# Kernel optimization log

Measured on AMD Instinct MI355X. Metric: run time of the kernel, lower is better.

The kernel has to match this reference:

```python
import jax, jax.numpy as jnp
import numpy as np

L, H, D, A, T = 2, 8, 512, 64, 256  # layers, heads, model_dim, attention_dim, target_dim
B, S = 2, 2048
EPS = 1e-5


def _ln(x, g, b):
    m = jnp.mean(x, axis=-1, keepdims=True)
    v = jnp.mean((x - m) ** 2, axis=-1, keepdims=True)
    return (x - m) / jnp.sqrt(v + EPS) * g + b


def setup_inputs() -> dict:
    key = jax.random.key(0)
    ks = jax.random.split(key, 16)
    s = 0.02
    inp = {
        "x": jax.random.normal(ks[0], (B, S, D), jnp.float32),
        # per-head QKV projections, stacked over layers and heads
        "Wq": jax.random.normal(ks[1], (L, H, D, A), jnp.float32) * s,
        "bq": jnp.zeros((L, H, A), jnp.float32),
        "Wk": jax.random.normal(ks[2], (L, H, D, A), jnp.float32) * s,
        "bk": jnp.zeros((L, H, A), jnp.float32),
        "Wv": jax.random.normal(ks[3], (L, H, D, A), jnp.float32) * s,
        "bv": jnp.zeros((L, H, A), jnp.float32),
        # output projection of concatenated heads: [H*A, D]
        "Wo": jax.random.normal(ks[4], (L, H * A, D), jnp.float32) * s,
        "bo": jnp.zeros((L, D), jnp.float32),
        # AddNorm after attention
        "ln1_g": jnp.ones((L, D), jnp.float32),
        "ln1_b": jnp.zeros((L, D), jnp.float32),
        # FFN (hidden_dim == model_dim in this module)
        "W1": jax.random.normal(ks[5], (L, D, D), jnp.float32) * s,
        "b1": jnp.zeros((L, D), jnp.float32),
        "W2": jax.random.normal(ks[6], (L, D, D), jnp.float32) * s,
        "b2": jnp.zeros((L, D), jnp.float32),
        # AddNorm after FFN
        "ln2_g": jnp.ones((L, D), jnp.float32),
        "ln2_b": jnp.zeros((L, D), jnp.float32),
        # final projection to target_dim
        "Wp": jax.random.normal(ks[7], (D, T), jnp.float32) * s,
        "bp": jnp.zeros((T,), jnp.float32),
    }
    return inp


def reference(x, Wq, bq, Wk, bk, Wv, bv, Wo, bo, ln1_g, ln1_b,
              W1, b1, W2, b2, ln2_g, ln2_b, Wp, bp):
    scale = 1.0 / jnp.sqrt(jnp.asarray(A, x.dtype))
    for i in range(L):
        # batched per-head QKV projections (math identical to per-head Linears)
        q = jnp.einsum('bsd,hda->bhsa', x, Wq[i]) + bq[i][:, None, :]
        k = jnp.einsum('bsd,hda->bhsa', x, Wk[i]) + bk[i][:, None, :]
        v = jnp.einsum('bsd,hda->bhsa', x, Wv[i]) + bv[i][:, None, :]
        scores = jnp.einsum('bhsa,bhta->bhst', q, k) * scale  # [B,H,S,S]
        attn = jax.nn.softmax(scores, axis=-1)
        heads = jnp.einsum('bhst,bhta->bhsa', attn, v)        # [B,H,S,A]
        concat = heads.transpose(0, 2, 1, 3).reshape(x.shape[0], x.shape[1], H * A)
        mha = concat @ Wo[i] + bo[i]
        x = _ln(x + mha, ln1_g[i], ln1_b[i])
        ffn = jax.nn.relu(x @ W1[i] + b1[i]) @ W2[i] + b2[i]
        x = _ln(x + ffn, ln2_g[i], ln2_b[i])
    return x @ Wp + bp
```

## Files before the change

### kernel.cpp

```cpp
#include <hip/hip_runtime.h>
#include <hip/hip_bf16.h>

#define MDIM 4096
#define DDIM 512
#define HHEADS 8
#define SLEN 2048
#define TDIM 256
#define SPLIT 4
#define LDT 66
#define LDA 66
#define EXPC 0.1803368801111244f

typedef __attribute__((ext_vector_type(8))) short short8;
typedef __attribute__((ext_vector_type(16))) float f32x16;

__device__ __forceinline__ unsigned short f2bf(float f) {
    union { __hip_bfloat16 h; unsigned short u; } c;
    c.h = __float2bfloat16(f);
    return c.u;
}
__device__ __forceinline__ float bf2f(short s) {
    return __uint_as_float((unsigned)(unsigned short)s << 16);
}

__global__ __launch_bounds__(256) void prep_k(
    const float* __restrict__ Wq, const float* __restrict__ Wk, const float* __restrict__ Wv,
    const float* __restrict__ Wo, const float* __restrict__ W1, const float* __restrict__ W2,
    const float* __restrict__ Wp, const float* __restrict__ x,
    short* __restrict__ Wqt, short* __restrict__ Wkt, short* __restrict__ Wvt,
    short* __restrict__ Wot, short* __restrict__ W1t, short* __restrict__ W2t,
    short* __restrict__ Wpt, short* __restrict__ xbf)
{
    __shared__ short T[64][72];
    const int b = blockIdx.x, tid = threadIdx.x;

    if (b >= 800) {
        const int idx = (b - 800) * 256 + tid;
        for (int e = idx; e < 262144; e += 65536) {
            float4 f0 = *(const float4*)&x[e * 8];
            float4 f1 = *(const float4*)&x[e * 8 + 4];
            short8 o;
            o[0] = (short)f2bf(f0.x); o[1] = (short)f2bf(f0.y);
            o[2] = (short)f2bf(f0.z); o[3] = (short)f2bf(f0.w);
            o[4] = (short)f2bf(f1.x); o[5] = (short)f2bf(f1.y);
            o[6] = (short)f2bf(f1.z); o[7] = (short)f2bf(f1.w);
            *(short8*)&xbf[e * 8] = o;
        }
        return;
    }

    const float* srcp; short* dstp; int ss;
    if (b < 384) {
        int w = b >> 7, t = b & 127;
        int lh = t >> 3, kt0 = (t & 7) << 6;
        const float* W = (w == 0) ? Wq : (w == 1) ? Wk : Wv;
        short* Wt = (w == 0) ? Wqt : (w == 1) ? Wkt : Wvt;
        srcp = W + (size_t)lh * 32768 + (size_t)kt0 * 64;
        dstp = Wt + (size_t)lh * 32768 + kt0;
        ss = 64;
    } else if (b < 768) {
        int w = (b - 384) >> 7, t = (b - 384) & 127;
        int l = t >> 6, tt = t & 63;
        int kt0 = (tt >> 3) << 6, nt0 = (tt & 7) << 6;
        const float* W = (w == 0) ? Wo : (w == 1) ? W1 : W2;
        short* Wt = (w == 0) ? Wot : (w == 1) ? W1t : W2t;
        srcp = W + (size_t)l * 262144 + (size_t)kt0 * 512 + nt0;
        dstp = Wt + (size_t)l * 262144 + (size_t)nt0 * 512 + kt0;
        ss = 512;
    } else {
        int t = b - 768;
        int kt0 = (t >> 2) << 6, nt0 = (t & 3) << 6;
        srcp = Wp + (size_t)kt0 * 256 + nt0;
        dstp = Wpt + (size_t)nt0 * 512 + kt0;
        ss = 256;
    }

    const int r = tid >> 2, c0 = (tid & 3) * 16;
#pragma unroll
    for (int j = 0; j < 16; j += 4) {
        float4 f = *(const float4*)&srcp[(size_t)r * ss + c0 + j];
        T[r][c0 + j + 0] = (short)f2bf(f.x);
        T[r][c0 + j + 1] = (short)f2bf(f.y);
        T[r][c0 + j + 2] = (short)f2bf(f.z);
        T[r][c0 + j + 3] = (short)f2bf(f.w);
    }
    __syncthreads();
    short8 o0, o1;
#pragma unroll
    for (int j = 0; j < 8; ++j) { o0[j] = T[c0 + j][r]; o1[j] = T[c0 + 8 + j][r]; }
    *(short8*)&dstp[(size_t)r * 512 + c0] = o0;
    *(short8*)&dstp[(size_t)r * 512 + c0 + 8] = o1;
}

__global__ __launch_bounds__(256, 2) void gemm_bf(
    const short* __restrict__ A, const short* __restrict__ Bt,
    const float* __restrict__ bias, void* __restrict__ Cout,
    int M, int N, int K, int flags)
{
    __shared__ short As[64 * LDT];
    __shared__ short Bs[64 * LDT];
    const int tid = threadIdx.x;
    const int wave = tid >> 6, lane = tid & 63;
    const int l31 = lane & 31, hi = lane >> 5;
    const int wm = wave >> 1, wn = wave & 1;
    const int m0 = blockIdx.y * 64, n0 = blockIdx.x * 64;

    f32x16 acc;
#pragma unroll
    for (int r = 0; r < 16; ++r) acc[r] = 0.f;

    const int sr = tid >> 2;
    const int sc = (tid & 3) * 16;

    for (int k0 = 0; k0 < K; k0 += 64) {
        __syncthreads();
        *(short8*)&As[sr * LDT + sc]     = *(const short8*)&A[(size_t)(m0 + sr) * K + k0 + sc];
        *(short8*)&As[sr * LDT + sc + 8] = *(const short8*)&A[(size_t)(m0 + sr) * K + k0 + sc + 8];
        *(short8*)&Bs[sr * LDT + sc]     = *(const short8*)&Bt[(size_t)(n0 + sr) * K + k0 + sc];
        *(short8*)&Bs[sr * LDT + sc + 8] = *(const short8*)&Bt[(size_t)(n0 + sr) * K + k0 + sc + 8];
        __syncthreads();

        short8 af[4], bfm[4];
#pragma unroll
        for (int ks = 0; ks < 4; ++ks) {
            af[ks]  = *(const short8*)&As[(wm * 32 + l31) * LDT + ks * 16 + hi * 8];
            bfm[ks] = *(const short8*)&Bs[(wn * 32 + l31) * LDT + ks * 16 + hi * 8];
        }
#pragma unroll
        for (int ks = 0; ks < 4; ++ks)
            acc = __builtin_amdgcn_mfma_f32_32x32x16_bf16(af[ks], bfm[ks], acc, 0, 0, 0);
    }

    const int col = n0 + wn * 32 + l31;
    const float bb = bias[col];
    const int rbase = m0 + wm * 32 + 4 * hi;
#pragma unroll
    for (int r = 0; r < 16; ++r) {
        int row = rbase + (r & 3) + 8 * (r >> 2);
        float v = acc[r] + bb;
        if (flags & 1) v = fmaxf(v, 0.f);
        if (flags & 2) ((short*)Cout)[(size_t)row * N + col] = (short)f2bf(v);
        else           ((float*)Cout)[(size_t)row * N + col] = v;
    }
}

__global__ __launch_bounds__(256, 2) void qkv_bf(
    const short* __restrict__ A,
    const short* __restrict__ Wqt, const short* __restrict__ Wkt, const short* __restrict__ Wvt,
    const float* __restrict__ bq, const float* __restrict__ bk, const float* __restrict__ bv,
    short* __restrict__ Oq, short* __restrict__ Ok, short* __restrict__ Ov)
{
    __shared__ short As[128 * LDT];
    __shared__ short Bs[64 * LDT];
    const int tid = threadIdx.x;
    const int wave = tid >> 6, lane = tid & 63;
    const int l31 = lane & 31, hi = lane >> 5;
    const int wm = wave >> 1, wn = wave & 1;
    const int m0 = blockIdx.y * 128;
    const int nt = blockIdx.x;
    const int which = nt >> 3, h = nt & 7;

    const short* Bt = ((which == 0) ? Wqt : (which == 1) ? Wkt : Wvt) + (size_t)h * 64 * 512;
    const float* bias = ((which == 0) ? bq : (which == 1) ? bk : bv) + h * 64;
    short* Out = (which == 0) ? Oq : (which == 1) ? Ok : Ov;

    f32x16 acc[2];
#pragma unroll
    for (int ms = 0; ms < 2; ++ms)
#pragma unroll
        for (int r = 0; r < 16; ++r) acc[ms][r] = 0.f;

    const int sr = tid >> 3;
    const int sc = (tid & 7) * 8;

    for (int k0 = 0; k0 < 512; k0 += 64) {
        __syncthreads();
#pragma unroll
        for (int p = 0; p < 4; ++p)
            *(short8*)&As[(p * 32 + sr) * LDT + sc] =
                *(const short8*)&A[(size_t)(m0 + p * 32 + sr) * 512 + k0 + sc];
#pragma unroll
        for (int p = 0; p < 2; ++p)
            *(short8*)&Bs[(p * 32 + sr) * LDT + sc] =
                *(const short8*)&Bt[(size_t)(p * 32 + sr) * 512 + k0 + sc];
        __syncthreads();

        short8 af[2][4], bfm[4];
#pragma unroll
        for (int ms = 0; ms < 2; ++ms)
#pragma unroll
            for (int ks = 0; ks < 4; ++ks)
                af[ms][ks] = *(const short8*)&As[(wm * 64 + ms * 32 + l31) * LDT + ks * 16 + hi * 8];
#pragma unroll
        for (int ks = 0; ks < 4; ++ks)
            bfm[ks] = *(const short8*)&Bs[(wn * 32 + l31) * LDT + ks * 16 + hi * 8];
#pragma unroll
        for (int ms = 0; ms < 2; ++ms)
#pragma unroll
            for (int ks = 0; ks < 4; ++ks)
                acc[ms] = __builtin_amdgcn_mfma_f32_32x32x16_bf16(af[ms][ks], bfm[ks], acc[ms], 0, 0, 0);
    }

    const int a = wn * 32 + l31;
    const float bb = bias[a];
    const int b = m0 >> 11;
    const int sb = (m0 & (SLEN - 1)) + wm * 64;
    const int bh = b * HHEADS + h;

    if (which == 0) {
        short* Ob = Out + (size_t)bh * SLEN * 64;
#pragma unroll
        for (int ms = 0; ms < 2; ++ms)
#pragma unroll
            for (int r = 0; r < 16; ++r) {
                int s = sb + ms * 32 + (r & 3) + 8 * (r >> 2) + 4 * hi;
                Ob[(size_t)s * 64 + a] = (short)f2bf((acc[ms][r] + bb) * EXPC);
            }
    } else if (which == 1) {
        short* Ob = Out + (size_t)bh * SLEN * 64;
#pragma unroll
        for (int ms = 0; ms < 2; ++ms)
#pragma unroll
            for (int r = 0; r < 16; ++r) {
                int s = sb + ms * 32 + (r & 3) + 8 * (r >> 2) + 4 * hi;
                Ob[(size_t)s * 64 + a] = (short)f2bf(acc[ms][r] + bb);
            }
    } else {
        short* Ob = Out + ((size_t)bh * 64 + a) * SLEN;
#pragma unroll
        for (int ms = 0; ms < 2; ++ms)
#pragma unroll
            for (int g = 0; g < 4; ++g) {
                int s = sb + ms * 32 + 8 * g + 4 * hi;
                ushort4 w;
                w.x = f2bf(acc[ms][4 * g + 0] + bb);
                w.y = f2bf(acc[ms][4 * g + 1] + bb);
                w.z = f2bf(acc[ms][4 * g + 2] + bb);
                w.w = f2bf(acc[ms][4 * g + 3] + bb);
                *(ushort4*)&Ob[s] = w;
            }
    }
}

__global__ __launch_bounds__(256, 2) void attn_mfma(
    const short* __restrict__ Qb, const short* __restrict__ Kb,
    const short* __restrict__ Vtb, short* __restrict__ Op,
    float* __restrict__ lp)
{
    __shared__ short Ks[64 * LDA];
    __shared__ short Vs[64 * LDA];

    const int tid = threadIdx.x;
    const int wid = tid >> 6;
    const int lane = tid & 63;
    const int l31 = lane & 31;
    const int hi = lane >> 5;

    const int qt = blockIdx.x;
    const int bh = blockIdx.y;
    const int sp = blockIdx.z;

    const short* Qg = Qb + (size_t)bh * SLEN * 64;
    const short* Kg = Kb + (size_t)bh * SLEN * 64;
    const short* Vg = Vtb + (size_t)bh * 64 * SLEN;

    const int q0 = qt * 256 + wid * 64;

    short8 qf[2][4];
#pragma unroll
    for (int nt = 0; nt < 2; ++nt)
#pragma unroll
        for (int ks = 0; ks < 4; ++ks)
            qf[nt][ks] = *(const short8*)&Qg[(size_t)(q0 + nt * 32 + l31) * 64 + ks * 16 + hi * 8];

    f32x16 oacc[2][2];
    float lsum[2] = {0.f, 0.f};
#pragma unroll
    for (int nt = 0; nt < 2; ++nt)
#pragma unroll
        for (int dt = 0; dt < 2; ++dt)
#pragma unroll
            for (int r = 0; r < 16; ++r) oacc[nt][dt][r] = 0.f;

    const int srow = tid >> 2;
    const int sch = (tid & 3) * 16;
    const int kbase = sp * (SLEN / SPLIT);

    short8 rk0 = *(const short8*)&Kg[(size_t)(kbase + srow) * 64 + sch];
    short8 rk1 = *(const short8*)&Kg[(size_t)(kbase + srow) * 64 + sch + 8];
    short8 rv0 = *(const short8*)&Vg[(size_t)srow * SLEN + kbase + sch];
    short8 rv1 = *(const short8*)&Vg[(size_t)srow * SLEN + kbase + sch + 8];

#pragma unroll 1
    for (int kt = 0; kt < 8; ++kt) {
        __syncthreads();
        *(short8*)&Ks[srow * LDA + sch]     = rk0;
        *(short8*)&Ks[srow * LDA + sch + 8] = rk1;
        *(short8*)&Vs[srow * LDA + sch]     = rv0;
        *(short8*)&Vs[srow * LDA + sch + 8] = rv1;
        __syncthreads();

        if (kt < 7) {
            const int k0n = kbase + (kt + 1) * 64;
            rk0 = *(const short8*)&Kg[(size_t)(k0n + srow) * 64 + sch];
            rk1 = *(const short8*)&Kg[(size_t)(k0n + srow) * 64 + sch + 8];
            rv0 = *(const short8*)&Vg[(size_t)srow * SLEN + k0n + sch];
            rv1 = *(const short8*)&Vg[(size_t)srow * SLEN + k0n + sch + 8];
        }

        short8 kf[2][4], vf[2][4];
#pragma unroll
        for (int mt = 0; mt < 2; ++mt)
#pragma unroll
            for (int ks = 0; ks < 4; ++ks)
                kf[mt][ks] = *(const short8*)&Ks[(mt * 32 + l31) * LDA + ks * 16 + hi * 8];
#pragma unroll
        for (int dt = 0; dt < 2; ++dt)
#pragma unroll
            for (int p = 0; p < 4; ++p)
                vf[dt][p] = *(const short8*)&Vs[(dt * 32 + l31) * LDA + p * 16 + hi * 8];

#pragma unroll
        for (int nt = 0; nt < 2; ++nt) {
            f32x16 sacc[2];
            __builtin_amdgcn_s_setprio(1);
#pragma unroll
            for (int mt = 0; mt < 2; ++mt) {
                f32x16 s;
#pragma unroll
                for (int r = 0; r < 16; ++r) s[r] = 0.f;
#pragma unroll
                for (int ks = 0; ks < 4; ++ks)
                    s = __builtin_amdgcn_mfma_f32_32x32x16_bf16(kf[mt][ks], qf[nt][ks], s, 0, 0, 0);
                sacc[mt] = s;
            }
            __builtin_amdgcn_s_setprio(0);

            int2 pk[2][4];
#pragma unroll
            for (int mt = 0; mt < 2; ++mt)
#pragma unroll
                for (int g = 0; g < 4; ++g) {
                    unsigned a0 = __float_as_uint(__builtin_amdgcn_exp2f(sacc[mt][4 * g + 0]));
                    unsigned a1 = __float_as_uint(__builtin_amdgcn_exp2f(sacc[mt][4 * g + 1]));
                    unsigned a2 = __float_as_uint(__builtin_amdgcn_exp2f(sacc[mt][4 * g + 2]));
                    unsigned a3 = __float_as_uint(__builtin_amdgcn_exp2f(sacc[mt][4 * g + 3]));
                    float t0 = __uint_as_float(a0 & 0xffff0000u);
                    float t1 = __uint_as_float(a1 & 0xffff0000u);
                    float t2 = __uint_as_float(a2 & 0xffff0000u);
                    float t3 = __uint_as_float(a3 & 0xffff0000u);
                    lsum[nt] += (t0 + t1) + (t2 + t3);
                    pk[mt][g].x = (int)__builtin_amdgcn_perm(a1, a0, 0x07060302u);
                    pk[mt][g].y = (int)__builtin_amdgcn_perm(a3, a2, 0x07060302u);
                }

            int2 xch[2][2];
#pragma unroll
            for (int mt = 0; mt < 2; ++mt)
#pragma unroll
                for (int h2 = 0; h2 < 2; ++h2) {
                    int2 v = hi ? pk[mt][2 * h2] : pk[mt][2 * h2 + 1];
                    xch[mt][h2].x = __shfl_xor(v.x, 32);
                    xch[mt][h2].y = __shfl_xor(v.y, 32);
                }

            __builtin_amdgcn_s_setprio(1);
#pragma unroll
            for (int p = 0; p < 4; ++p) {
                const int mt = p >> 1, h2 = p & 1;
                const int ga = 2 * h2, gb = 2 * h2 + 1;
                const int2 X = xch[mt][h2];
                union { int4 i; short8 s; } u;
                u.i.x = hi ? X.x : pk[mt][ga].x;
                u.i.y = hi ? X.y : pk[mt][ga].y;
                u.i.z = hi ? pk[mt][gb].x : X.x;
                u.i.w = hi ? pk[mt][gb].y : X.y;
#pragma unroll
                for (int dt = 0; dt < 2; ++dt)
                    oacc[nt][dt] = __builtin_amdgcn_mfma_f32_32x32x16_bf16(u.s, vf[dt][p], oacc[nt][dt], 0, 0, 0);
            }
            __builtin_amdgcn_s_setprio(0);
        }
    }

#pragma unroll
    for (int nt = 0; nt < 2; ++nt) {
        float lt = lsum[nt] + __shfl_xor(lsum[nt], 32);
        if (hi == 0)
            lp[((size_t)(sp * 16 + bh)) * SLEN + q0 + nt * 32 + l31] = lt;
#pragma unroll
        for (int dt = 0; dt < 2; ++dt) {
#pragma unroll
            for (int r = 0; r < 16; ++r) {
                int qrow = (r & 3) + 8 * (r >> 2) + 4 * hi;
                size_t addr = (((size_t)(sp * 16 + bh)) * SLEN + (q0 + nt * 32 + qrow)) * 64 + dt * 32 + l31;
                Op[addr] = (short)f2bf(oacc[nt][dt][r]);
            }
        }
    }
}

__global__ __launch_bounds__(256) void merge_k(
    const short* __restrict__ Op, const float* __restrict__ lp,
    short* __restrict__ hc)
{
    const int g = blockIdx.x * 256 + threadIdx.x;
    const int d4 = g & 15;
    const int s = (g >> 4) & (SLEN - 1);
    const int bh = g >> 15;

    float o[4] = {0.f, 0.f, 0.f, 0.f};
    float ls = 0.f;
#pragma unroll
    for (int sp = 0; sp < SPLIT; ++sp) {
        const size_t base = (((size_t)(sp * 16 + bh)) * SLEN + s);
        ushort4 u4 = *(const ushort4*)&Op[base * 64 + d4 * 4];
        o[0] += bf2f((short)u4.x); o[1] += bf2f((short)u4.y);
        o[2] += bf2f((short)u4.z); o[3] += bf2f((short)u4.w);
        ls += lp[base];
    }
    const int b = bh >> 3, h = bh & 7;
    const float inv = 1.f / ls;
    ushort4 w;
    w.x = f2bf(o[0] * inv); w.y = f2bf(o[1] * inv);
    w.z = f2bf(o[2] * inv); w.w = f2bf(o[3] * inv);
    *(ushort4*)&hc[((size_t)(b * SLEN + s)) * DDIM + h * 64 + d4 * 4] = w;
}

__global__ __launch_bounds__(256) void addnorm_bf(
    short* __restrict__ X, const float* __restrict__ Y,
    const float* __restrict__ g, const float* __restrict__ beta)
{
    const int lane = threadIdx.x & 63;
    const int t = blockIdx.x * 4 + (threadIdx.x >> 6);
    short* xr = X + (size_t)t * DDIM;
    const float* yr = Y + (size_t)t * DDIM;
    const int c0 = lane * 8;

    short8 x8 = *(const short8*)&xr[c0];
    float4 y0 = *(const float4*)&yr[c0];
    float4 y1 = *(const float4*)&yr[c0 + 4];
    float v[8];
    v[0] = bf2f(x8[0]) + y0.x; v[1] = bf2f(x8[1]) + y0.y;
    v[2] = bf2f(x8[2]) + y0.z; v[3] = bf2f(x8[3]) + y0.w;
    v[4] = bf2f(x8[4]) + y1.x; v[5] = bf2f(x8[5]) + y1.y;
    v[6] = bf2f(x8[6]) + y1.z; v[7] = bf2f(x8[7]) + y1.w;

    float s1 = 0.f, s2 = 0.f;
#pragma unroll
    for (int j = 0; j < 8; ++j) { s1 += v[j]; s2 += v[j] * v[j]; }
#pragma unroll
    for (int off = 1; off < 64; off <<= 1) {
        s1 += __shfl_xor(s1, off);
        s2 += __shfl_xor(s2, off);
    }
    float mean = s1 * (1.0f / DDIM);
    float var = s2 * (1.0f / DDIM) - mean * mean;
    float rstd = rsqrtf(var + 1e-5f);

    float4 ga = *(const float4*)&g[c0];
    float4 gb = *(const float4*)&g[c0 + 4];
    float4 ba = *(const float4*)&beta[c0];
    float4 bb = *(const float4*)&beta[c0 + 4];
    float gg[8] = {ga.x, ga.y, ga.z, ga.w, gb.x, gb.y, gb.z, gb.w};
    float bt[8] = {ba.x, ba.y, ba.z, ba.w, bb.x, bb.y, bb.z, bb.w};

    short8 o8;
#pragma unroll
    for (int j = 0; j < 8; ++j)
        o8[j] = (short)f2bf((v[j] - mean) * rstd * gg[j] + bt[j]);
    *(short8*)&xr[c0] = o8;
}

extern "C" void kernel_launch(void* const* d_in, const int* in_sizes, int n_in,
                              void* d_out, int out_size, void* d_ws, size_t ws_size,
                              hipStream_t stream)
{
    (void)in_sizes; (void)n_in; (void)out_size; (void)ws_size;
    const float* x   = (const float*)d_in[0];
    const float* Wq  = (const float*)d_in[1];
    const float* bq  = (const float*)d_in[2];
    const float* Wk  = (const float*)d_in[3];
    const float* bk  = (const float*)d_in[4];
    const float* Wv  = (const float*)d_in[5];
    const float* bv  = (const float*)d_in[6];
    const float* Wo  = (const float*)d_in[7];
    const float* bo  = (const float*)d_in[8];
    const float* g1  = (const float*)d_in[9];
    const float* be1 = (const float*)d_in[10];
    const float* W1  = (const float*)d_in[11];
    const float* b1  = (const float*)d_in[12];
    const float* W2  = (const float*)d_in[13];
    const float* b2  = (const float*)d_in[14];
    const float* g2  = (const float*)d_in[15];
    const float* be2 = (const float*)d_in[16];
    const float* Wp  = (const float*)d_in[17];
    const float* bp  = (const float*)d_in[18];

    char* wsb = (char*)d_ws;
    const size_t MB = 1024 * 1024;
    short* xbf   = (short*)(wsb + 0);
    short* Qbuf  = (short*)(wsb + 4 * MB);
    short* Kbuf  = (short*)(wsb + 8 * MB);
    short* Vtbuf = (short*)(wsb + 12 * MB);
    short* Opart = (short*)(wsb + 16 * MB);
    float* y     = (float*)(wsb + 16 * MB);
    short* hidbf = (short*)(wsb + 24 * MB);
    float* lpart = (float*)(wsb + 32 * MB);
    short* hcbf  = Qbuf;
    short* Wqt   = (short*)(wsb + 33 * MB);
    short* Wkt   = (short*)(wsb + 34 * MB);
    short* Wvt   = (short*)(wsb + 35 * MB);
    short* Wot   = (short*)(wsb + 36 * MB);
    short* W1t   = (short*)(wsb + 37 * MB);
    short* W2t   = (short*)(wsb + 38 * MB);
    short* Wpt   = (short*)(wsb + 39 * MB);

    prep_k<<<1056, 256, 0, stream>>>(Wq, Wk, Wv, Wo, W1, W2, Wp, x,
                                     Wqt, Wkt, Wvt, Wot, W1t, W2t, Wpt, xbf);

    for (int i = 0; i < 2; ++i) {
        const size_t wOff = (size_t)i * 262144;
        qkv_bf<<<dim3(24, 32), 256, 0, stream>>>(
            xbf, Wqt + wOff, Wkt + wOff, Wvt + wOff,
            bq + i * 512, bk + i * 512, bv + i * 512,
            Qbuf, Kbuf, Vtbuf);
        attn_mfma<<<dim3(8, 16, SPLIT), 256, 0, stream>>>(Qbuf, Kbuf, Vtbuf, Opart, lpart);
        merge_k<<<2048, 256, 0, stream>>>(Opart, lpart, hcbf);
        gemm_bf<<<dim3(8, 64), 256, 0, stream>>>(
            hcbf, Wot + wOff, bo + i * 512, y, MDIM, DDIM, DDIM, 0);
        addnorm_bf<<<1024, 256, 0, stream>>>(xbf, y, g1 + i * 512, be1 + i * 512);
        gemm_bf<<<dim3(8, 64), 256, 0, stream>>>(
            xbf, W1t + wOff, b1 + i * 512, hidbf, MDIM, DDIM, DDIM, 3);
        gemm_bf<<<dim3(8, 64), 256, 0, stream>>>(
            hidbf, W2t + wOff, b2 + i * 512, y, MDIM, DDIM, DDIM, 0);
        addnorm_bf<<<1024, 256, 0, stream>>>(xbf, y, g2 + i * 512, be2 + i * 512);
    }
    gemm_bf<<<dim3(4, 64), 256, 0, stream>>>(
        xbf, Wpt, bp, (float*)d_out, MDIM, TDIM, DDIM, 0);
}
```

Baseline: 282.3 us.

## Shrink attention query tile, swizzle block order, deepen GEMM K-step

```diff
diff --git a/kernel.cpp b/kernel.cpp
--- a/kernel.cpp
+++ b/kernel.cpp
@@ -9,6 +9,7 @@
 #define SPLIT 4
 #define LDT 66
 #define LDA 66
+#define LDG 130
 #define EXPC 0.1803368801111244f
 
 typedef __attribute__((ext_vector_type(8))) short short8;
@@ -97,8 +98,8 @@
     const float* __restrict__ bias, void* __restrict__ Cout,
     int M, int N, int K, int flags)
 {
-    __shared__ short As[64 * LDT];
-    __shared__ short Bs[64 * LDT];
+    __shared__ short As[64 * LDG];
+    __shared__ short Bs[64 * LDG];
     const int tid = threadIdx.x;
     const int wave = tid >> 6, lane = tid & 63;
     const int l31 = lane & 31, hi = lane >> 5;
@@ -110,24 +111,27 @@
     for (int r = 0; r < 16; ++r) acc[r] = 0.f;
 
     const int sr = tid >> 2;
-    const int sc = (tid & 3) * 16;
-
-    for (int k0 = 0; k0 < K; k0 += 64) {
+    const int sc = (tid & 3) * 32;
+
+    for (int k0 = 0; k0 < K; k0 += 128) {
         __syncthreads();
-        *(short8*)&As[sr * LDT + sc]     = *(const short8*)&A[(size_t)(m0 + sr) * K + k0 + sc];
-        *(short8*)&As[sr * LDT + sc + 8] = *(const short8*)&A[(size_t)(m0 + sr) * K + k0 + sc + 8];
-        *(short8*)&Bs[sr * LDT + sc]     = *(const short8*)&Bt[(size_t)(n0 + sr) * K + k0 + sc];
-        *(short8*)&Bs[sr * LDT + sc + 8] = *(const short8*)&Bt[(size_t)(n0 + sr) * K + k0 + sc + 8];
+#pragma unroll
+        for (int j = 0; j < 4; ++j) {
+            *(short8*)&As[sr * LDG + sc + j * 8] =
+                *(const short8*)&A[(size_t)(m0 + sr) * K + k0 + sc + j * 8];
+            *(short8*)&Bs[sr * LDG + sc + j * 8] =
+                *(const short8*)&Bt[(size_t)(n0 + sr) * K + k0 + sc + j * 8];
+        }
         __syncthreads();
 
-        short8 af[4], bfm[4];
-#pragma unroll
-        for (int ks = 0; ks < 4; ++ks) {
-            af[ks]  = *(const short8*)&As[(wm * 32 + l31) * LDT + ks * 16 + hi * 8];
-            bfm[ks] = *(const short8*)&Bs[(wn * 32 + l31) * LDT + ks * 16 + hi * 8];
-        }
-#pragma unroll
-        for (int ks = 0; ks < 4; ++ks)
+        short8 af[8], bfm[8];
+#pragma unroll
+        for (int ks = 0; ks < 8; ++ks) {
+            af[ks]  = *(const short8*)&As[(wm * 32 + l31) * LDG + ks * 16 + hi * 8];
+            bfm[ks] = *(const short8*)&Bs[(wn * 32 + l31) * LDG + ks * 16 + hi * 8];
+        }
+#pragma unroll
+        for (int ks = 0; ks < 8; ++ks)
             acc = __builtin_amdgcn_mfma_f32_32x32x16_bf16(af[ks], bfm[ks], acc, 0, 0, 0);
     }
 
@@ -242,7 +246,7 @@
     }
 }
 
-__global__ __launch_bounds__(256, 2) void attn_mfma(
+__global__ __launch_bounds__(256, 4) void attn_mfma(
     const short* __restrict__ Qb, const short* __restrict__ Kb,
     const short* __restrict__ Vtb, short* __restrict__ Op,
     float* __restrict__ lp)
@@ -256,31 +260,27 @@
     const int l31 = lane & 31;
     const int hi = lane >> 5;
 
-    const int qt = blockIdx.x;
-    const int bh = blockIdx.y;
-    const int sp = blockIdx.z;
+    const int bidx = blockIdx.x;
+    const int swz = (bidx & 7) * 128 + (bidx >> 3);
+    const int sp = swz & 3, qt = (swz >> 2) & 15, bh = swz >> 6;
 
     const short* Qg = Qb + (size_t)bh * SLEN * 64;
     const short* Kg = Kb + (size_t)bh * SLEN * 64;
     const short* Vg = Vtb + (size_t)bh * 64 * SLEN;
 
-    const int q0 = qt * 256 + wid * 64;
-
-    short8 qf[2][4];
-#pragma unroll
-    for (int nt = 0; nt < 2; ++nt)
-#pragma unroll
-        for (int ks = 0; ks < 4; ++ks)
-            qf[nt][ks] = *(const short8*)&Qg[(size_t)(q0 + nt * 32 + l31) * 64 + ks * 16 + hi * 8];
-
-    f32x16 oacc[2][2];
-    float lsum[2] = {0.f, 0.f};
-#pragma unroll
-    for (int nt = 0; nt < 2; ++nt)
-#pragma unroll
-        for (int dt = 0; dt < 2; ++dt)
-#pragma unroll
-            for (int r = 0; r < 16; ++r) oacc[nt][dt][r] = 0.f;
+    const int q0 = qt * 128 + wid * 32;
+
+    short8 qf[4];
+#pragma unroll
+    for (int ks = 0; ks < 4; ++ks)
+        qf[ks] = *(const short8*)&Qg[(size_t)(q0 + l31) * 64 + ks * 16 + hi * 8];
+
+    f32x16 oacc[2];
+    float lsum = 0.f;
+#pragma unroll
+    for (int dt = 0; dt < 2; ++dt)
+#pragma unroll
+        for (int r = 0; r < 16; ++r) oacc[dt][r] = 0.f;
 
     const int srow = tid >> 2;
     const int sch = (tid & 3) * 16;
@@ -320,82 +320,76 @@
             for (int p = 0; p < 4; ++p)
                 vf[dt][p] = *(const short8*)&Vs[(dt * 32 + l31) * LDA + p * 16 + hi * 8];
 
-#pragma unroll
-        for (int nt = 0; nt < 2; ++nt) {
-            f32x16 sacc[2];
-            __builtin_amdgcn_s_setprio(1);
-#pragma unroll
-            for (int mt = 0; mt < 2; ++mt) {
-                f32x16 s;
-#pragma unroll
-                for (int r = 0; r < 16; ++r) s[r] = 0.f;
-#pragma unroll
-                for (int ks = 0; ks < 4; ++ks)
-                    s = __builtin_amdgcn_mfma_f32_32x32x16_bf16(kf[mt][ks], qf[nt][ks], s, 0, 0, 0);
-                sacc[mt] = s;
+        f32x16 sacc[2];
+        __builtin_amdgcn_s_setprio(1);
+#pragma unroll
+        for (int mt = 0; mt < 2; ++mt) {
+            f32x16 s;
+#pragma unroll
+            for (int r = 0; r < 16; ++r) s[r] = 0.f;
+#pragma unroll
+            for (int ks = 0; ks < 4; ++ks)
+                s = __builtin_amdgcn_mfma_f32_32x32x16_bf16(kf[mt][ks], qf[ks], s, 0, 0, 0);
+            sacc[mt] = s;
+        }
+        __builtin_amdgcn_s_setprio(0);
+
+        int2 pk[2][4];
+#pragma unroll
+        for (int mt = 0; mt < 2; ++mt)
+#pragma unroll
+            for (int g = 0; g < 4; ++g) {
+                unsigned a0 = __float_as_uint(__builtin_amdgcn_exp2f(sacc[mt][4 * g + 0]));
+                unsigned a1 = __float_as_uint(__builtin_amdgcn_exp2f(sacc[mt][4 * g + 1]));
+                unsigned a2 = __float_as_uint(__builtin_amdgcn_exp2f(sacc[mt][4 * g + 2]));
+                unsigned a3 = __float_as_uint(__builtin_amdgcn_exp2f(sacc[mt][4 * g + 3]));
+                float t0 = __uint_as_float(a0 & 0xffff0000u);
+                float t1 = __uint_as_float(a1 & 0xffff0000u);
+                float t2 = __uint_as_float(a2 & 0xffff0000u);
+                float t3 = __uint_as_float(a3 & 0xffff0000u);
+                lsum += (t0 + t1) + (t2 + t3);
+                pk[mt][g].x = (int)__builtin_amdgcn_perm(a1, a0, 0x07060302u);
+                pk[mt][g].y = (int)__builtin_amdgcn_perm(a3, a2, 0x07060302u);
             }
-            __builtin_amdgcn_s_setprio(0);
-
-            int2 pk[2][4];
-#pragma unroll
-            for (int mt = 0; mt < 2; ++mt)
-#pragma unroll
-                for (int g = 0; g < 4; ++g) {
-                    unsigned a0 = __float_as_uint(__builtin_amdgcn_exp2f(sacc[mt][4 * g + 0]));
-                    unsigned a1 = __float_as_uint(__builtin_amdgcn_exp2f(sacc[mt][4 * g + 1]));
-                    unsigned a2 = __float_as_uint(__builtin_amdgcn_exp2f(sacc[mt][4 * g + 2]));
-                    unsigned a3 = __float_as_uint(__builtin_amdgcn_exp2f(sacc[mt][4 * g + 3]));
-                    float t0 = __uint_as_float(a0 & 0xffff0000u);
-                    float t1 = __uint_as_float(a1 & 0xffff0000u);
-                    float t2 = __uint_as_float(a2 & 0xffff0000u);
-                    float t3 = __uint_as_float(a3 & 0xffff0000u);
-                    lsum[nt] += (t0 + t1) + (t2 + t3);
-                    pk[mt][g].x = (int)__builtin_amdgcn_perm(a1, a0, 0x07060302u);
-                    pk[mt][g].y = (int)__builtin_amdgcn_perm(a3, a2, 0x07060302u);
-                }
-
-            int2 xch[2][2];
-#pragma unroll
-            for (int mt = 0; mt < 2; ++mt)
-#pragma unroll
-                for (int h2 = 0; h2 < 2; ++h2) {
-                    int2 v = hi ? pk[mt][2 * h2] : pk[mt][2 * h2 + 1];
-                    xch[mt][h2].x = __shfl_xor(v.x, 32);
-                    xch[mt][h2].y = __shfl_xor(v.y, 32);
-                }
-
-            __builtin_amdgcn_s_setprio(1);
-#pragma unroll
-            for (int p = 0; p < 4; ++p) {
-                const int mt = p >> 1, h2 = p & 1;
-                const int ga = 2 * h2, gb = 2 * h2 + 1;
-                const int2 X = xch[mt][h2];
-                union { int4 i; short8 s; } u;
-                u.i.x = hi ? X.x : pk[mt][ga].x;
-                u.i.y = hi ? X.y : pk[mt][ga].y;
-                u.i.z = hi ? pk[mt][gb].x : X.x;
-                u.i.w = hi ? pk[mt][gb].y : X.y;
-#pragma unroll
-                for (int dt = 0; dt < 2; ++dt)
-                    oacc[nt][dt] = __builtin_amdgcn_mfma_f32_32x32x16_bf16(u.s, vf[dt][p], oacc[nt][dt], 0, 0, 0);
+
+        int2 xch[2][2];
+#pragma unroll
+        for (int mt = 0; mt < 2; ++mt)
+#pragma unroll
+            for (int h2 = 0; h2 < 2; ++h2) {
+                int2 v = hi ? pk[mt][2 * h2] : pk[mt][2 * h2 + 1];
+                xch[mt][h2].x = __shfl_xor(v.x, 32);
+                xch[mt][h2].y = __shfl_xor(v.y, 32);
             }
-            __builtin_amdgcn_s_setprio(0);
-        }
-    }
-
-#pragma unroll
-    for (int nt = 0; nt < 2; ++nt) {
-        float lt = lsum[nt] + __shfl_xor(lsum[nt], 32);
-        if (hi == 0)
-            lp[((size_t)(sp * 16 + bh)) * SLEN + q0 + nt * 32 + l31] = lt;
-#pragma unroll
-        for (int dt = 0; dt < 2; ++dt) {
-#pragma unroll
-            for (int r = 0; r < 16; ++r) {
-                int qrow = (r & 3) + 8 * (r >> 2) + 4 * hi;
-                size_t addr = (((size_t)(sp * 16 + bh)) * SLEN + (q0 + nt * 32 + qrow)) * 64 + dt * 32 + l31;
-                Op[addr] = (short)f2bf(oacc[nt][dt][r]);
-            }
+
+        __builtin_amdgcn_s_setprio(1);
+#pragma unroll
+        for (int p = 0; p < 4; ++p) {
+            const int mt = p >> 1, h2 = p & 1;
+            const int ga = 2 * h2, gb = 2 * h2 + 1;
+            const int2 X = xch[mt][h2];
+            union { int4 i; short8 s; } u;
+            u.i.x = hi ? X.x : pk[mt][ga].x;
+            u.i.y = hi ? X.y : pk[mt][ga].y;
+            u.i.z = hi ? pk[mt][gb].x : X.x;
+            u.i.w = hi ? pk[mt][gb].y : X.y;
+#pragma unroll
+            for (int dt = 0; dt < 2; ++dt)
+                oacc[dt] = __builtin_amdgcn_mfma_f32_32x32x16_bf16(u.s, vf[dt][p], oacc[dt], 0, 0, 0);
+        }
+        __builtin_amdgcn_s_setprio(0);
+    }
+
+    const float lt = lsum + __shfl_xor(lsum, 32);
+    if (hi == 0)
+        lp[((size_t)(sp * 16 + bh)) * SLEN + q0 + l31] = lt;
+#pragma unroll
+    for (int dt = 0; dt < 2; ++dt) {
+#pragma unroll
+        for (int r = 0; r < 16; ++r) {
+            int qrow = (r & 3) + 8 * (r >> 2) + 4 * hi;
+            size_t addr = (((size_t)(sp * 16 + bh)) * SLEN + (q0 + qrow)) * 64 + dt * 32 + l31;
+            Op[addr] = (short)f2bf(oacc[dt][r]);
         }
     }
 }
@@ -525,7 +519,7 @@
             xbf, Wqt + wOff, Wkt + wOff, Wvt + wOff,
             bq + i * 512, bk + i * 512, bv + i * 512,
             Qbuf, Kbuf, Vtbuf);
-        attn_mfma<<<dim3(8, 16, SPLIT), 256, 0, stream>>>(Qbuf, Kbuf, Vtbuf, Opart, lpart);
+        attn_mfma<<<1024, 256, 0, stream>>>(Qbuf, Kbuf, Vtbuf, Opart, lpart);
         merge_k<<<2048, 256, 0, stream>>>(Opart, lpart, hcbf);
         gemm_bf<<<dim3(8, 64), 256, 0, stream>>>(
             hcbf, Wot + wOff, bo + i * 512, y, MDIM, DDIM, DDIM, 0);
```

Measured after the change: 376.3 us. +33.3%, slower.
